# Kernel optimization log

Hardware: AMD Instinct MI355X
Metric: run time of the kernel (lower is better)

## Reference

```python
import jax, jax.numpy as jnp
import numpy as np

B, H, LQ, LK, D = 2, 16, 2048, 2048, 128

def setup_inputs() -> dict:
    key = jax.random.key(0)
    k1, k2, k3 = jax.random.split(key, 3)
    q = jax.random.normal(k1, (B, H, LQ, D), dtype=jnp.float32)
    k = jax.random.normal(k2, (B, H, LK, D), dtype=jnp.float32)
    v = jax.random.normal(k3, (B, H, LK, D), dtype=jnp.float32)
    return {"q": q, "k": k, "v": v}

def reference(q, k, v):
    # scaled dot-product attention: softmax(q k^T / sqrt(D)) v
    scale = q.shape[-1] ** (-0.5)
    # scores: [B,H,Lq,Lk]
    scores = jnp.einsum('bhqd,bhkd->bhqk', q, k) * scale
    attn = jax.nn.softmax(scores, axis=-1)
    out = jnp.einsum('bhqk,bhkd->bhqd', attn, v)  # [B,H,Lq,Dv]
    return out
```

## Files before the change

### kernel.cpp

```cpp
#include <hip/hip_runtime.h>
#include <hip/hip_bf16.h>
#include <cstdint>

#define LQ_N   2048
#define LK_N   2048
#define DD     128
#define NHEADS 32
#define QBLK   128
#define KVBLK  64
#define NKV    (LK_N / KVBLK)
#define NQB    (LQ_N / QBLK)
#define SCALE  0.08838834764831845f
#define SCALE2 0.1275525003267101f

#define KTILE_BYTES (KVBLK * DD * 2)
#define WS_K_BYTES  ((size_t)NHEADS * NKV * KTILE_BYTES)
#define WS_NEED     (2 * WS_K_BYTES)

#define KB_OFF(b)   ((b) * KTILE_BYTES)
#define VB_OFF(s)   (2 * KTILE_BYTES + (s) * KTILE_BYTES)
#define SMEM_MAIN   (5 * KTILE_BYTES)

#define PSTR 72

typedef __attribute__((ext_vector_type(8)))  short bf16x8;
typedef __attribute__((ext_vector_type(4)))  float f32x4;
typedef __attribute__((ext_vector_type(16))) float f32x16;

#if __has_builtin(__builtin_amdgcn_exp2f)
#define EXP2F __builtin_amdgcn_exp2f
#else
#define EXP2F exp2f
#endif

__device__ inline unsigned short f2bf(float f) {
    union { float f; unsigned u; } x; x.f = f;
    unsigned r = (x.u + 0x7fffu + ((x.u >> 16) & 1u)) >> 16;
    return (unsigned short)r;
}

__device__ inline unsigned cvt_pk_bf16(float lo, float hi) {
    unsigned r;
    asm("v_cvt_pk_bf16_f32 %0, %1, %2" : "=v"(r) : "v"(lo), "v"(hi));
    return r;
}

__device__ inline bf16x8 make_pfrag(float v0, float v1, float v2, float v3,
                                    float v4, float v5, float v6, float v7) {
    unsigned a0 = cvt_pk_bf16(v0, v1);
    unsigned a1 = cvt_pk_bf16(v2, v3);
    unsigned b0 = cvt_pk_bf16(v4, v5);
    unsigned b1 = cvt_pk_bf16(v6, v7);
    asm volatile("v_permlane32_swap_b32 %0, %1" : "+v"(a0), "+v"(b0));
    asm volatile("v_permlane32_swap_b32 %0, %1" : "+v"(a1), "+v"(b1));
    union { unsigned u[4]; bf16x8 v8; } u;
    u.u[0] = a0; u.u[1] = a1; u.u[2] = b0; u.u[3] = b1;
    return u.v8;
}

__device__ inline void gld16(const char* g, const char* l) {
    __builtin_amdgcn_global_load_lds(
        (const __attribute__((address_space(1))) unsigned int*)g,
        (__attribute__((address_space(3))) unsigned int*)l,
        16, 0, 0);
}

__global__ __launch_bounds__(256, 2)
void prep_k_kernel(const float* __restrict__ K, char* __restrict__ ws)
{
    __shared__ unsigned short kt[KVBLK * 136];
    const int tid  = threadIdx.x;
    const int kvt  = blockIdx.x;
    const int head = blockIdx.y;
    const float* Kh = K + ((size_t)head * LK_N + (size_t)kvt * KVBLK) * DD;
    #pragma unroll
    for (int i = 0; i < 4; ++i) {
        int c = tid + 256 * i;
        int r  = c >> 4;
        int c8 = c & 15;
        const float* src = Kh + (size_t)r * DD + c8 * 8;
        float4 a = *(const float4*)src;
        float4 b = *(const float4*)(src + 4);
        bf16x8 t;
        t[0] = (short)f2bf(a.x * SCALE2); t[1] = (short)f2bf(a.y * SCALE2);
        t[2] = (short)f2bf(a.z * SCALE2); t[3] = (short)f2bf(a.w * SCALE2);
        t[4] = (short)f2bf(b.x * SCALE2); t[5] = (short)f2bf(b.y * SCALE2);
        t[6] = (short)f2bf(b.z * SCALE2); t[7] = (short)f2bf(b.w * SCALE2);
        *(bf16x8*)&kt[r * 136 + c8 * 8] = t;
    }
    __syncthreads();
    char* dst = ws + ((size_t)head * NKV + kvt) * KTILE_BYTES;
    #pragma unroll
    for (int i = 0; i < 4; ++i) {
        int c = tid + 256 * i;
        int g = c >> 6;
        int r = c & 63;
        bf16x8 t = *(const bf16x8*)&kt[r * 136 + g * 8];
        *(bf16x8*)(dst + c * 16) = t;
    }
}

__global__ __launch_bounds__(256, 2)
void prep_vt_kernel(const float* __restrict__ V, char* __restrict__ ws)
{
    __shared__ unsigned short vt[DD * PSTR];
    const int tid  = threadIdx.x;
    const int kvt  = blockIdx.x;
    const int head = blockIdx.y;
    const float* Vh = V + ((size_t)head * LK_N + (size_t)kvt * KVBLK) * DD;
    #pragma unroll
    for (int i = 0; i < 8; ++i) {
        int f = tid + 256 * i;
        int r  = f >> 5;
        int c4 = f & 31;
        float4 x = *(const float4*)(Vh + (size_t)r * DD + c4 * 4);
        vt[(c4 * 4 + 0) * PSTR + r] = f2bf(x.x);
        vt[(c4 * 4 + 1) * PSTR + r] = f2bf(x.y);
        vt[(c4 * 4 + 2) * PSTR + r] = f2bf(x.z);
        vt[(c4 * 4 + 3) * PSTR + r] = f2bf(x.w);
    }
    __syncthreads();
    char* dst = ws + WS_K_BYTES + ((size_t)head * NKV + kvt) * KTILE_BYTES;
    #pragma unroll
    for (int i = 0; i < 4; ++i) {
        int c = tid + 256 * i;
        int g = c >> 7;
        int d = c & 127;
        bf16x8 t = *(const bf16x8*)&vt[d * PSTR + g * 8];
        *(bf16x8*)(dst + c * 16) = t;
    }
}

__global__ __launch_bounds__(256, 2)
void attn_main_kernel(const float* __restrict__ Q, const char* __restrict__ kws,
                      const char* __restrict__ vws, float* __restrict__ O)
{
    extern __shared__ char smem[];

    const int tid  = threadIdx.x;
    const int lane = tid & 63;
    const int wave = tid >> 6;
    const int l31  = lane & 31;
    const int h    = lane >> 5;

    const int bid  = blockIdx.x;
    const int sid  = (bid & 7) * (NQB * NHEADS / 8) + (bid >> 3);
    const int head = sid >> 4;
    const int qb   = sid & 15;

    const float* Qh = Q + (size_t)head * LQ_N * DD;
    float*       Oh = O + (size_t)head * LQ_N * DD;
    const char*  kt_g = kws + (size_t)head * NKV * KTILE_BYTES;
    const char*  vt_g = vws + (size_t)head * NKV * KTILE_BYTES;

    const int qrow = qb * QBLK + wave * 32 + l31;
    bf16x8 qf[8];
    {
        const float* qp = Qh + (size_t)qrow * DD + 8 * h;
        #pragma unroll
        for (int kd = 0; kd < 8; ++kd) {
            float4 a = *(const float4*)(qp + 16 * kd);
            float4 b = *(const float4*)(qp + 16 * kd + 4);
            bf16x8 t;
            t[0] = (short)f2bf(a.x); t[1] = (short)f2bf(a.y);
            t[2] = (short)f2bf(a.z); t[3] = (short)f2bf(a.w);
            t[4] = (short)f2bf(b.x); t[5] = (short)f2bf(b.y);
            t[6] = (short)f2bf(b.z); t[7] = (short)f2bf(b.w);
            qf[kd] = t;
        }
    }
    asm volatile("s_waitcnt vmcnt(0)" ::: "memory");

    f32x16 o_acc[4];
    #pragma unroll
    for (int nt = 0; nt < 4; ++nt)
        #pragma unroll
        for (int i = 0; i < 16; ++i) o_acc[nt][i] = 0.f;
    float m_run = -1e30f, l_run = 0.f;

    auto issue = [&](int t) {
        const char* ks = kt_g + (size_t)t * KTILE_BYTES;
        const char* vs = vt_g + (size_t)t * KTILE_BYTES;
        const char* kl = smem + KB_OFF(t & 1);
        const char* vl = smem + VB_OFF(t % 3);
        #pragma unroll
        for (int i = 0; i < 4; ++i) {
            int off = (tid + 256 * i) * 16;
            gld16(ks + off, kl + off);
            gld16(vs + off, vl + off);
        }
    };

    auto do_qk = [&](f32x16& s0, f32x16& s1, const char* kb) {
        #pragma unroll
        for (int i = 0; i < 16; ++i) { s0[i] = 0.f; s1[i] = 0.f; }
        __builtin_amdgcn_s_setprio(1);
        #pragma unroll
        for (int kd = 0; kd < 8; ++kd) {
            int g = 2 * kd + h;
            bf16x8 kf0 = *(const bf16x8*)(kb + ((g * 64 + l31) << 4));
            bf16x8 kf1 = *(const bf16x8*)(kb + ((g * 64 + 32 + l31) << 4));
            s0 = __builtin_amdgcn_mfma_f32_32x32x16_bf16(kf0, qf[kd], s0, 0, 0, 0);
            s1 = __builtin_amdgcn_mfma_f32_32x32x16_bf16(kf1, qf[kd], s1, 0, 0, 0);
        }
        __builtin_amdgcn_s_setprio(0);
    };

    auto do_smpv = [&](f32x16& s0, f32x16& s1, const char* vb) {
        float pmax = s0[0];
        #pragma unroll
        for (int i = 1; i < 16; ++i) pmax = fmaxf(pmax, s0[i]);
        #pragma unroll
        for (int i = 0; i < 16; ++i) pmax = fmaxf(pmax, s1[i]);
        pmax = fmaxf(pmax, __shfl_xor(pmax, 32));

        if (!__all(pmax <= m_run + 8.0f)) {
            float mn = fmaxf(m_run, pmax);
            float al = EXP2F(m_run - mn);
            m_run = mn;
            l_run *= al;
            #pragma unroll
            for (int nt = 0; nt < 4; ++nt)
                #pragma unroll
                for (int i = 0; i < 16; ++i) o_acc[nt][i] *= al;
        }
        float sum = 0.f;
        #pragma unroll
        for (int i = 0; i < 16; ++i) { s0[i] = EXP2F(s0[i] - m_run); sum += s0[i]; }
        #pragma unroll
        for (int i = 0; i < 16; ++i) { s1[i] = EXP2F(s1[i] - m_run); sum += s1[i]; }
        sum += __shfl_xor(sum, 32);
        l_run += sum;

        bf16x8 pf0 = make_pfrag(s0[0], s0[1], s0[2],  s0[3],  s0[4],  s0[5],  s0[6],  s0[7]);
        bf16x8 pf1 = make_pfrag(s0[8], s0[9], s0[10], s0[11], s0[12], s0[13], s0[14], s0[15]);
        bf16x8 pf2 = make_pfrag(s1[0], s1[1], s1[2],  s1[3],  s1[4],  s1[5],  s1[6],  s1[7]);
        bf16x8 pf3 = make_pfrag(s1[8], s1[9], s1[10], s1[11], s1[12], s1[13], s1[14], s1[15]);

        __builtin_amdgcn_s_setprio(1);
        #pragma unroll
        for (int nt = 0; nt < 4; ++nt) {
            int d = 32 * nt + l31;
            bf16x8 vf0 = *(const bf16x8*)(vb + (((0 + h) * 128 + d) << 4));
            bf16x8 vf1 = *(const bf16x8*)(vb + (((2 + h) * 128 + d) << 4));
            bf16x8 vf2 = *(const bf16x8*)(vb + (((4 + h) * 128 + d) << 4));
            bf16x8 vf3 = *(const bf16x8*)(vb + (((6 + h) * 128 + d) << 4));
            o_acc[nt] = __builtin_amdgcn_mfma_f32_32x32x16_bf16(vf0, pf0, o_acc[nt], 0, 0, 0);
            o_acc[nt] = __builtin_amdgcn_mfma_f32_32x32x16_bf16(vf1, pf1, o_acc[nt], 0, 0, 0);
            o_acc[nt] = __builtin_amdgcn_mfma_f32_32x32x16_bf16(vf2, pf2, o_acc[nt], 0, 0, 0);
            o_acc[nt] = __builtin_amdgcn_mfma_f32_32x32x16_bf16(vf3, pf3, o_acc[nt], 0, 0, 0);
        }
        __builtin_amdgcn_s_setprio(0);
    };

    f32x16 sA0, sA1, sB0, sB1;

    issue(0);
    issue(1);

    asm volatile("s_waitcnt vmcnt(8)" ::: "memory");
    __builtin_amdgcn_s_barrier();
    do_qk(sA0, sA1, smem + KB_OFF(0));
    __builtin_amdgcn_s_barrier();
    issue(2);

    for (int t = 1; t < NKV - 1; t += 2) {
        asm volatile("s_waitcnt vmcnt(8)" ::: "memory");
        __builtin_amdgcn_s_barrier();
        do_qk(sB0, sB1, smem + KB_OFF(1));
        do_smpv(sA0, sA1, smem + VB_OFF((t - 1) % 3));
        __builtin_amdgcn_s_barrier();
        issue(t + 2);

        asm volatile("s_waitcnt vmcnt(8)" ::: "memory");
        __builtin_amdgcn_s_barrier();
        do_qk(sA0, sA1, smem + KB_OFF(0));
        do_smpv(sB0, sB1, smem + VB_OFF(t % 3));
        __builtin_amdgcn_s_barrier();
        if (t + 3 < NKV) issue(t + 3);
    }

    asm volatile("s_waitcnt vmcnt(0)" ::: "memory");
    __builtin_amdgcn_s_barrier();
    do_qk(sB0, sB1, smem + KB_OFF(1));
    do_smpv(sA0, sA1, smem + VB_OFF((NKV - 2) % 3));
    do_smpv(sB0, sB1, smem + VB_OFF((NKV - 1) % 3));

    float inv = 1.0f / l_run;
    float* op = Oh + (size_t)qrow * DD;
    #pragma unroll
    for (int nt = 0; nt < 4; ++nt)
        #pragma unroll
        for (int p = 0; p < 4; ++p) {
            int dbase = 32 * nt + 8 * p + 4 * h;
            float4 w;
            w.x = o_acc[nt][4 * p + 0] * inv;
            w.y = o_acc[nt][4 * p + 1] * inv;
            w.z = o_acc[nt][4 * p + 2] * inv;
            w.w = o_acc[nt][4 * p + 3] * inv;
            *(float4*)(op + dbase) = w;
        }
}

#define KSTRIDE  136
#define VTSTRIDE 40
#define FKV 32

__global__ __launch_bounds__(256, 2)
void attn_fwd_fallback(const float* __restrict__ Q, const float* __restrict__ K,
                       const float* __restrict__ V, float* __restrict__ O)
{
    __shared__ unsigned short k_lds[FKV * KSTRIDE];
    __shared__ unsigned short vt_lds[DD * VTSTRIDE];
    __shared__ unsigned short p_lds2[4 * 16 * VTSTRIDE];

    const int tid  = threadIdx.x;
    const int lane = tid & 63;
    const int wave = tid >> 6;
    const int head = blockIdx.y;
    const int qb   = blockIdx.x;

    const float* Qh = Q + (size_t)head * LQ_N * DD;
    const float* Kh = K + (size_t)head * LK_N * DD;
    const float* Vh = V + (size_t)head * LK_N * DD;
    float*       Oh = O + (size_t)head * LQ_N * DD;

    const int r16 = lane & 15;
    const int g   = lane >> 4;

    const int qrow = qb * 64 + wave * 16 + r16;
    bf16x8 qf[4];
    {
        const float* qp = Qh + (size_t)qrow * DD + 8 * g;
        #pragma unroll
        for (int kt = 0; kt < 4; ++kt) {
            float4 a = *(const float4*)(qp + 32 * kt);
            float4 b = *(const float4*)(qp + 32 * kt + 4);
            bf16x8 t;
            t[0] = (short)f2bf(a.x * SCALE); t[1] = (short)f2bf(a.y * SCALE);
            t[2] = (short)f2bf(a.z * SCALE); t[3] = (short)f2bf(a.w * SCALE);
            t[4] = (short)f2bf(b.x * SCALE); t[5] = (short)f2bf(b.y * SCALE);
            t[6] = (short)f2bf(b.z * SCALE); t[7] = (short)f2bf(b.w * SCALE);
            qf[kt] = t;
        }
    }

    f32x4 o_acc[8];
    #pragma unroll
    for (int dt = 0; dt < 8; ++dt) o_acc[dt] = (f32x4){0.f, 0.f, 0.f, 0.f};
    float m_run[4], l_run[4];
    #pragma unroll
    for (int r = 0; r < 4; ++r) { m_run[r] = -1e30f; l_run[r] = 0.f; }

    for (int kv = 0; kv < LK_N / FKV; ++kv) {
        const float* Kt = Kh + (size_t)kv * FKV * DD;
        const float* Vt = Vh + (size_t)kv * FKV * DD;
        __syncthreads();
        #pragma unroll
        for (int i = 0; i < 4; ++i) {
            int f = tid + 256 * i;
            int row = f >> 5, colf = f & 31;
            float4 x = *(const float4*)(Kt + (size_t)row * DD + colf * 4);
            ushort4 pk;
            pk.x = f2bf(x.x); pk.y = f2bf(x.y); pk.z = f2bf(x.z); pk.w = f2bf(x.w);
            *(ushort4*)(&k_lds[row * KSTRIDE + colf * 4]) = pk;
        }
        #pragma unroll
        for (int i = 0; i < 4; ++i) {
            int f = tid + 256 * i;
            int row = f >> 5, colf = f & 31;
            float4 x = *(const float4*)(Vt + (size_t)row * DD + colf * 4);
            vt_lds[(colf * 4 + 0) * VTSTRIDE + row] = f2bf(x.x);
            vt_lds[(colf * 4 + 1) * VTSTRIDE + row] = f2bf(x.y);
            vt_lds[(colf * 4 + 2) * VTSTRIDE + row] = f2bf(x.z);
            vt_lds[(colf * 4 + 3) * VTSTRIDE + row] = f2bf(x.w);
        }
        __syncthreads();

        f32x4 s0 = (f32x4){0.f,0.f,0.f,0.f};
        f32x4 s1 = (f32x4){0.f,0.f,0.f,0.f};
        #pragma unroll
        for (int kt = 0; kt < 4; ++kt) {
            bf16x8 kf0 = *(const bf16x8*)&k_lds[(r16)      * KSTRIDE + 32 * kt + 8 * g];
            bf16x8 kf1 = *(const bf16x8*)&k_lds[(16 + r16) * KSTRIDE + 32 * kt + 8 * g];
            s0 = __builtin_amdgcn_mfma_f32_16x16x32_bf16(qf[kt], kf0, s0, 0, 0, 0);
            s1 = __builtin_amdgcn_mfma_f32_16x16x32_bf16(qf[kt], kf1, s1, 0, 0, 0);
        }

        float alpha[4];
        f32x4 p0, p1;
        #pragma unroll
        for (int r = 0; r < 4; ++r) {
            float t = fmaxf(s0[r], s1[r]);
            t = fmaxf(t, __shfl_xor(t, 1));
            t = fmaxf(t, __shfl_xor(t, 2));
            t = fmaxf(t, __shfl_xor(t, 4));
            t = fmaxf(t, __shfl_xor(t, 8));
            float mn = fmaxf(m_run[r], t);
            alpha[r] = __expf(m_run[r] - mn);
            m_run[r] = mn;
            p0[r] = __expf(s0[r] - mn);
            p1[r] = __expf(s1[r] - mn);
            float su = p0[r] + p1[r];
            su += __shfl_xor(su, 1);
            su += __shfl_xor(su, 2);
            su += __shfl_xor(su, 4);
            su += __shfl_xor(su, 8);
            l_run[r] = l_run[r] * alpha[r] + su;
        }

        unsigned short* pw = &p_lds2[wave * 16 * VTSTRIDE];
        #pragma unroll
        for (int r = 0; r < 4; ++r) {
            int row = 4 * g + r;
            pw[row * VTSTRIDE + r16]      = f2bf(p0[r]);
            pw[row * VTSTRIDE + 16 + r16] = f2bf(p1[r]);
        }
        bf16x8 pf = *(const bf16x8*)&pw[r16 * VTSTRIDE + 8 * g];

        #pragma unroll
        for (int dt = 0; dt < 8; ++dt) {
            #pragma unroll
            for (int r = 0; r < 4; ++r) o_acc[dt][r] *= alpha[r];
        }
        #pragma unroll
        for (int dt = 0; dt < 8; ++dt) {
            bf16x8 vf = *(const bf16x8*)&vt_lds[(16 * dt + r16) * VTSTRIDE + 8 * g];
            o_acc[dt] = __builtin_amdgcn_mfma_f32_16x16x32_bf16(pf, vf, o_acc[dt], 0, 0, 0);
        }
    }

    #pragma unroll
    for (int r = 0; r < 4; ++r) {
        float inv = 1.0f / l_run[r];
        int row = qb * 64 + wave * 16 + 4 * g + r;
        float* op = Oh + (size_t)row * DD + r16;
        #pragma unroll
        for (int dt = 0; dt < 8; ++dt)
            op[16 * dt] = o_acc[dt][r] * inv;
    }
}

extern "C" void kernel_launch(void* const* d_in, const int* in_sizes, int n_in,
                              void* d_out, int out_size, void* d_ws, size_t ws_size,
                              hipStream_t stream) {
    const float* q = (const float*)d_in[0];
    const float* k = (const float*)d_in[1];
    const float* v = (const float*)d_in[2];
    float* o = (float*)d_out;

    hipError_t attr_ok = hipFuncSetAttribute(
        (const void*)attn_main_kernel,
        hipFuncAttributeMaxDynamicSharedMemorySize, SMEM_MAIN);

    if (ws_size >= WS_NEED && attr_ok == hipSuccess) {
        char* ws = (char*)d_ws;
        prep_k_kernel <<<dim3(NKV, NHEADS), 256, 0, stream>>>(k, ws);
        prep_vt_kernel<<<dim3(NKV, NHEADS), 256, 0, stream>>>(v, ws);
        attn_main_kernel<<<dim3(NQB * NHEADS), 256, SMEM_MAIN, stream>>>(
            q, ws, ws + WS_K_BYTES, o);
    } else {
        attn_fwd_fallback<<<dim3(LQ_N / 64, NHEADS), 256, 0, stream>>>(q, k, v, o);
    }
}
```

Before: 100.8 us.

## Interleave softmax max reduction with QK MFMAs and stream exp into PV rounds

Merges the QK^T step for the next tile with the softmax and PV step for the previous tile. The row-max reduction is placed between the QK MFMA issues, and each 8-element exp/convert chunk feeds its PV MFMAs right away. The aim is to hide VALU softmax work under MFMA latency and to shorten the live ranges of the exponentiated scores. It also drops the setprio calls, removes volatile from the permlane asm, and reorders the sum and PV accumulation, which may change register pressure and the instruction order the compiler chooses.

Measured after the change: 101.6 us. Within noise of the previous version (+0.8%).

```diff
diff --git a/kernel.cpp b/kernel.cpp
--- a/kernel.cpp
+++ b/kernel.cpp
@@ -33,6 +33,8 @@
 #define EXP2F exp2f
 #endif
 
+#define MFMA32(a, b, c) __builtin_amdgcn_mfma_f32_32x32x16_bf16((a), (b), (c), 0, 0, 0)
+
 __device__ inline unsigned short f2bf(float f) {
     union { float f; unsigned u; } x; x.f = f;
     unsigned r = (x.u + 0x7fffu + ((x.u >> 16) & 1u)) >> 16;
@@ -43,6 +45,10 @@
     unsigned r;
     asm("v_cvt_pk_bf16_f32 %0, %1, %2" : "=v"(r) : "v"(lo), "v"(hi));
     return r;
+}
+
+__device__ inline float fmax4(float a, float b, float c, float d) {
+    return fmaxf(fmaxf(a, b), fmaxf(c, d));
 }
 
 __device__ inline bf16x8 make_pfrag(float v0, float v1, float v2, float v3,
@@ -51,8 +57,8 @@
     unsigned a1 = cvt_pk_bf16(v2, v3);
     unsigned b0 = cvt_pk_bf16(v4, v5);
     unsigned b1 = cvt_pk_bf16(v6, v7);
-    asm volatile("v_permlane32_swap_b32 %0, %1" : "+v"(a0), "+v"(b0));
-    asm volatile("v_permlane32_swap_b32 %0, %1" : "+v"(a1), "+v"(b1));
+    asm("v_permlane32_swap_b32 %0, %1" : "+v"(a0), "+v"(b0));
+    asm("v_permlane32_swap_b32 %0, %1" : "+v"(a1), "+v"(b1));
     union { unsigned u[4]; bf16x8 v8; } u;
     u.u[0] = a0; u.u[1] = a1; u.u[2] = b0; u.u[3] = b1;
     return u.v8;
@@ -191,31 +197,31 @@
         }
     };
 
-    auto do_qk = [&](f32x16& s0, f32x16& s1, const char* kb) {
-        #pragma unroll
-        for (int i = 0; i < 16; ++i) { s0[i] = 0.f; s1[i] = 0.f; }
-        __builtin_amdgcn_s_setprio(1);
-        #pragma unroll
-        for (int kd = 0; kd < 8; ++kd) {
-            int g = 2 * kd + h;
-            bf16x8 kf0 = *(const bf16x8*)(kb + ((g * 64 + l31) << 4));
-            bf16x8 kf1 = *(const bf16x8*)(kb + ((g * 64 + 32 + l31) << 4));
-            s0 = __builtin_amdgcn_mfma_f32_32x32x16_bf16(kf0, qf[kd], s0, 0, 0, 0);
-            s1 = __builtin_amdgcn_mfma_f32_32x32x16_bf16(kf1, qf[kd], s1, 0, 0, 0);
-        }
-        __builtin_amdgcn_s_setprio(0);
-    };
-
-    auto do_smpv = [&](f32x16& s0, f32x16& s1, const char* vb) {
-        float pmax = s0[0];
-        #pragma unroll
-        for (int i = 1; i < 16; ++i) pmax = fmaxf(pmax, s0[i]);
-        #pragma unroll
-        for (int i = 0; i < 16; ++i) pmax = fmaxf(pmax, s1[i]);
-        pmax = fmaxf(pmax, __shfl_xor(pmax, 32));
-
-        if (!__all(pmax <= m_run + 8.0f)) {
-            float mn = fmaxf(m_run, pmax);
+#define QK_STEP(c0, c1, kb, kd) { \
+    bf16x8 kf0 = *(const bf16x8*)((kb) + (((2 * (kd) + h) * 64 + l31) << 4)); \
+    bf16x8 kf1 = *(const bf16x8*)((kb) + (((2 * (kd) + h) * 64 + 32 + l31) << 4)); \
+    c0 = MFMA32(kf0, qf[kd], c0); \
+    c1 = MFMA32(kf1, qf[kd], c1); }
+
+#define PV_ROUND(S, B, KS) { \
+    float e0 = EXP2F(S[B + 0] - m_run), e1 = EXP2F(S[B + 1] - m_run); \
+    float e2 = EXP2F(S[B + 2] - m_run), e3 = EXP2F(S[B + 3] - m_run); \
+    float e4 = EXP2F(S[B + 4] - m_run), e5 = EXP2F(S[B + 5] - m_run); \
+    float e6 = EXP2F(S[B + 6] - m_run), e7 = EXP2F(S[B + 7] - m_run); \
+    sum += ((e0 + e1) + (e2 + e3)) + ((e4 + e5) + (e6 + e7)); \
+    bf16x8 pf = make_pfrag(e0, e1, e2, e3, e4, e5, e6, e7); \
+    bf16x8 vf0 = *(const bf16x8*)(vb + (((2 * (KS) + h) * 128 +  0 + l31) << 4)); \
+    bf16x8 vf1 = *(const bf16x8*)(vb + (((2 * (KS) + h) * 128 + 32 + l31) << 4)); \
+    bf16x8 vf2 = *(const bf16x8*)(vb + (((2 * (KS) + h) * 128 + 64 + l31) << 4)); \
+    bf16x8 vf3 = *(const bf16x8*)(vb + (((2 * (KS) + h) * 128 + 96 + l31) << 4)); \
+    o_acc[0] = MFMA32(vf0, pf, o_acc[0]); \
+    o_acc[1] = MFMA32(vf1, pf, o_acc[1]); \
+    o_acc[2] = MFMA32(vf2, pf, o_acc[2]); \
+    o_acc[3] = MFMA32(vf3, pf, o_acc[3]); }
+
+    auto smpv_core = [&](f32x16& p0, f32x16& p1, const char* vb, float pm) {
+        if (!__all(pm <= m_run + 8.0f)) {
+            float mn = fmaxf(m_run, pm);
             float al = EXP2F(m_run - mn);
             m_run = mn;
             l_run *= al;
@@ -225,32 +231,54 @@
                 for (int i = 0; i < 16; ++i) o_acc[nt][i] *= al;
         }
         float sum = 0.f;
-        #pragma unroll
-        for (int i = 0; i < 16; ++i) { s0[i] = EXP2F(s0[i] - m_run); sum += s0[i]; }
-        #pragma unroll
-        for (int i = 0; i < 16; ++i) { s1[i] = EXP2F(s1[i] - m_run); sum += s1[i]; }
+        PV_ROUND(p0, 0, 0);
+        PV_ROUND(p0, 8, 1);
+        PV_ROUND(p1, 0, 2);
+        PV_ROUND(p1, 8, 3);
         sum += __shfl_xor(sum, 32);
         l_run += sum;
-
-        bf16x8 pf0 = make_pfrag(s0[0], s0[1], s0[2],  s0[3],  s0[4],  s0[5],  s0[6],  s0[7]);
-        bf16x8 pf1 = make_pfrag(s0[8], s0[9], s0[10], s0[11], s0[12], s0[13], s0[14], s0[15]);
-        bf16x8 pf2 = make_pfrag(s1[0], s1[1], s1[2],  s1[3],  s1[4],  s1[5],  s1[6],  s1[7]);
-        bf16x8 pf3 = make_pfrag(s1[8], s1[9], s1[10], s1[11], s1[12], s1[13], s1[14], s1[15]);
-
-        __builtin_amdgcn_s_setprio(1);
-        #pragma unroll
-        for (int nt = 0; nt < 4; ++nt) {
-            int d = 32 * nt + l31;
-            bf16x8 vf0 = *(const bf16x8*)(vb + (((0 + h) * 128 + d) << 4));
-            bf16x8 vf1 = *(const bf16x8*)(vb + (((2 + h) * 128 + d) << 4));
-            bf16x8 vf2 = *(const bf16x8*)(vb + (((4 + h) * 128 + d) << 4));
-            bf16x8 vf3 = *(const bf16x8*)(vb + (((6 + h) * 128 + d) << 4));
-            o_acc[nt] = __builtin_amdgcn_mfma_f32_32x32x16_bf16(vf0, pf0, o_acc[nt], 0, 0, 0);
-            o_acc[nt] = __builtin_amdgcn_mfma_f32_32x32x16_bf16(vf1, pf1, o_acc[nt], 0, 0, 0);
-            o_acc[nt] = __builtin_amdgcn_mfma_f32_32x32x16_bf16(vf2, pf2, o_acc[nt], 0, 0, 0);
-            o_acc[nt] = __builtin_amdgcn_mfma_f32_32x32x16_bf16(vf3, pf3, o_acc[nt], 0, 0, 0);
-        }
-        __builtin_amdgcn_s_setprio(0);
+    };
+
+    auto fused = [&](f32x16& c0, f32x16& c1, const char* kb,
+                     f32x16& p0, f32x16& p1, const char* vb) {
+        #pragma unroll
+        for (int i = 0; i < 16; ++i) { c0[i] = 0.f; c1[i] = 0.f; }
+        float x0, x1, x2, x3, y0, y1, y2, y3, pm;
+        QK_STEP(c0, c1, kb, 0); x0 = fmax4(p0[0],  p0[1],  p0[2],  p0[3]);
+        QK_STEP(c0, c1, kb, 1); x1 = fmax4(p0[4],  p0[5],  p0[6],  p0[7]);
+        QK_STEP(c0, c1, kb, 2); x2 = fmax4(p0[8],  p0[9],  p0[10], p0[11]);
+        QK_STEP(c0, c1, kb, 3); x3 = fmax4(p0[12], p0[13], p0[14], p0[15]);
+        QK_STEP(c0, c1, kb, 4); y0 = fmax4(p1[0],  p1[1],  p1[2],  p1[3]);
+                                y1 = fmax4(p1[4],  p1[5],  p1[6],  p1[7]);
+        QK_STEP(c0, c1, kb, 5); y2 = fmax4(p1[8],  p1[9],  p1[10], p1[11]);
+                                y3 = fmax4(p1[12], p1[13], p1[14], p1[15]);
+        QK_STEP(c0, c1, kb, 6); x0 = fmaxf(fmaxf(x0, x1), fmaxf(x2, x3));
+        QK_STEP(c0, c1, kb, 7); y0 = fmaxf(fmaxf(y0, y1), fmaxf(y2, y3));
+        pm = fmaxf(x0, y0);
+        pm = fmaxf(pm, __shfl_xor(pm, 32));
+        smpv_core(p0, p1, vb, pm);
+    };
+
+    auto qk_only = [&](f32x16& c0, f32x16& c1, const char* kb) {
+        #pragma unroll
+        for (int i = 0; i < 16; ++i) { c0[i] = 0.f; c1[i] = 0.f; }
+        #pragma unroll
+        for (int kd = 0; kd < 8; ++kd) QK_STEP(c0, c1, kb, kd);
+    };
+
+    auto smpv_only = [&](f32x16& p0, f32x16& p1, const char* vb) {
+        float x0 = fmax4(p0[0],  p0[1],  p0[2],  p0[3]);
+        float x1 = fmax4(p0[4],  p0[5],  p0[6],  p0[7]);
+        float x2 = fmax4(p0[8],  p0[9],  p0[10], p0[11]);
+        float x3 = fmax4(p0[12], p0[13], p0[14], p0[15]);
+        float y0 = fmax4(p1[0],  p1[1],  p1[2],  p1[3]);
+        float y1 = fmax4(p1[4],  p1[5],  p1[6],  p1[7]);
+        float y2 = fmax4(p1[8],  p1[9],  p1[10], p1[11]);
+        float y3 = fmax4(p1[12], p1[13], p1[14], p1[15]);
+        float pm = fmaxf(fmaxf(fmaxf(x0, x1), fmaxf(x2, x3)),
+                         fmaxf(fmaxf(y0, y1), fmaxf(y2, y3)));
+        pm = fmaxf(pm, __shfl_xor(pm, 32));
+        smpv_core(p0, p1, vb, pm);
     };
 
     f32x16 sA0, sA1, sB0, sB1;
@@ -260,31 +288,28 @@
 
     asm volatile("s_waitcnt vmcnt(8)" ::: "memory");
     __builtin_amdgcn_s_barrier();
-    do_qk(sA0, sA1, smem + KB_OFF(0));
+    qk_only(sA0, sA1, smem + KB_OFF(0));
     __builtin_amdgcn_s_barrier();
     issue(2);
 
     for (int t = 1; t < NKV - 1; t += 2) {
         asm volatile("s_waitcnt vmcnt(8)" ::: "memory");
         __builtin_amdgcn_s_barrier();
-        do_qk(sB0, sB1, smem + KB_OFF(1));
-        do_smpv(sA0, sA1, smem + VB_OFF((t - 1) % 3));
+        fused(sB0, sB1, smem + KB_OFF(1), sA0, sA1, smem + VB_OFF((t - 1) % 3));
         __builtin_amdgcn_s_barrier();
         issue(t + 2);
 
         asm volatile("s_waitcnt vmcnt(8)" ::: "memory");
         __builtin_amdgcn_s_barrier();
-        do_qk(sA0, sA1, smem + KB_OFF(0));
-        do_smpv(sB0, sB1, smem + VB_OFF(t % 3));
+        fused(sA0, sA1, smem + KB_OFF(0), sB0, sB1, smem + VB_OFF(t % 3));
         __builtin_amdgcn_s_barrier();
         if (t + 3 < NKV) issue(t + 3);
     }
 
     asm volatile("s_waitcnt vmcnt(0)" ::: "memory");
     __builtin_amdgcn_s_barrier();
-    do_qk(sB0, sB1, smem + KB_OFF(1));
-    do_smpv(sA0, sA1, smem + VB_OFF((NKV - 2) % 3));
-    do_smpv(sB0, sB1, smem + VB_OFF((NKV - 1) % 3));
+    fused(sB0, sB1, smem + KB_OFF(1), sA0, sA1, smem + VB_OFF((NKV - 2) % 3));
+    smpv_only(sB0, sB1, smem + VB_OFF((NKV - 1) % 3));
 
     float inv = 1.0f / l_run;
     float* op = Oh + (size_t)qrow * DD;
@@ -300,6 +325,8 @@
             w.w = o_acc[nt][4 * p + 3] * inv;
             *(float4*)(op + dbase) = w;
         }
+#undef QK_STEP
+#undef PV_ROUND
 }
 
 #define KSTRIDE  136
```
